# Optimization experiments

Measured on AMD Instinct MI355X. Metric: run time of the kernel, lower is better.

Reference implementation:

```python
import math
import jax, jax.numpy as jnp
import numpy as np

B, T, C = 2, 2048, 1024
N_HEAD = 16
HEAD_DIM = C // N_HEAD

def setup_inputs() -> dict:
    key = jax.random.key(0)
    kx, kq, kk, kv, kp = jax.random.split(key, 5)
    s = 1.0 / math.sqrt(C)
    return {
        "x": jax.random.normal(kx, (B, T, C), dtype=jnp.float32),
        "Wq": jax.random.normal(kq, (C, C), dtype=jnp.float32) * s,
        "Wk": jax.random.normal(kk, (C, C), dtype=jnp.float32) * s,
        "Wv": jax.random.normal(kv, (C, C), dtype=jnp.float32) * s,
        "Wproj": jax.random.normal(kp, (C, C), dtype=jnp.float32) * s,
    }

def reference(x, Wq, Wk, Wv, Wproj):
    b, t, c = x.shape
    # nn.Linear(no bias): x @ W.T ; weights stored [out, in]
    def heads(w):
        return (x @ w.T).reshape(b, t, N_HEAD, HEAD_DIM).transpose(0, 2, 1, 3)  # [B,H,T,D]
    q, k, v = heads(Wq), heads(Wk), heads(Wv)
    att = jnp.einsum('bhqd,bhkd->bhqk', q, k) / math.sqrt(HEAD_DIM)  # [B,H,T,T]
    causal = jnp.tril(jnp.ones((t, t), dtype=bool))
    att = jnp.where(causal, att, -jnp.inf)
    att = jax.nn.softmax(att, axis=-1)
    y = jnp.einsum('bhqk,bhkd->bhqd', att, v)           # [B,H,T,D]
    y = y.transpose(0, 2, 1, 3).reshape(b, t, c)        # [B,T,C]
    return y @ Wproj.T
```

## Files before the change

kernel.cpp:

```cpp
#include <hip/hip_runtime.h>
#include <stdint.h>

typedef uint16_t u16;
typedef uint32_t u32;
typedef __attribute__((ext_vector_type(8))) _Float16 f16x8;
typedef __attribute__((ext_vector_type(4))) float f32x4;

#define NB 2
#define NT 2048
#define NC 1024
#define NH 16
#define ND 64
#define NM (NB*NT)
#define LOG2E 1.44269504088896340736f

__device__ __forceinline__ u16 f2h(float f) {
  _Float16 h = (_Float16)f;
  return __builtin_bit_cast(u16, h);
}

__global__ __launch_bounds__(256) void cvt_kernel(const float* __restrict__ src,
                                                  u16* __restrict__ dst, int n4) {
  int i = blockIdx.x * 256 + threadIdx.x;
  if (i >= n4) return;
  float4 v = ((const float4*)src)[i];
  ushort4 o;
  o.x = f2h(v.x); o.y = f2h(v.y); o.z = f2h(v.z); o.w = f2h(v.w);
  ((ushort4*)dst)[i] = o;
}

__global__ __launch_bounds__(256) void cvtw_kernel(const float* __restrict__ w0,
                                                   const float* __restrict__ w1,
                                                   const float* __restrict__ w2,
                                                   const float* __restrict__ w3,
                                                   u16* __restrict__ dst) {
  int i = blockIdx.x * 256 + threadIdx.x;
  int which = i >> 18;
  const float* src = (which == 0) ? w0 : (which == 1) ? w1 : (which == 2) ? w2 : w3;
  int j = i & 262143;
  float4 v = ((const float4*)src)[j];
  ushort4 o;
  o.x = f2h(v.x); o.y = f2h(v.y); o.z = f2h(v.z); o.w = f2h(v.w);
  ((ushort4*)dst)[i] = o;
}

__device__ __forceinline__ void gload16(const void* g, void* l) {
  __builtin_amdgcn_global_load_lds(
      (const __attribute__((address_space(1))) void*)g,
      (__attribute__((address_space(3))) void*)l, 16, 0, 0);
}

template<int EPI>
__global__ __launch_bounds__(256) void gemm_bt(const u16* __restrict__ A,
                                               const u16* __restrict__ Bw,
                                               int K, int N,
                                               u16* __restrict__ oq, u16* __restrict__ okk,
                                               u16* __restrict__ ovt,
                                               float* __restrict__ of) {
  __shared__ __align__(16) u16 SH[2*128*64];
  u16* Al = SH;
  u16* Bl = SH + 128*64;
  const int tid = threadIdx.x, lane = tid & 63, wid = tid >> 6;
  const int g = lane >> 4, qq = lane & 15;
  const int wm = wid >> 1, wn = wid & 1;
  const int m0 = blockIdx.y * 128, n0 = blockIdx.x * 128;
  const int srow = lane >> 3;
  const int scol = (lane & 7) * 8;

  f32x4 acc[4][4] = {};

  for (int kt = 0; kt < K; kt += 64) {
    #pragma unroll
    for (int pp = 0; pp < 4; ++pp) {
      int r = wid*32 + pp*8;
      gload16(A  + (size_t)(m0 + r + srow)*K + kt + scol, &Al[r*64]);
      gload16(Bw + (size_t)(n0 + r + srow)*K + kt + scol, &Bl[r*64]);
    }
    __syncthreads();
    #pragma unroll
    for (int kk = 0; kk < 2; ++kk) {
      f16x8 af[4], bfr[4];
      #pragma unroll
      for (int mt = 0; mt < 4; ++mt)
        af[mt] = *(const f16x8*)&Al[(wm*64 + mt*16 + qq)*64 + kk*32 + 8*g];
      #pragma unroll
      for (int nt = 0; nt < 4; ++nt)
        bfr[nt] = *(const f16x8*)&Bl[(wn*64 + nt*16 + qq)*64 + kk*32 + 8*g];
      #pragma unroll
      for (int mt = 0; mt < 4; ++mt)
        #pragma unroll
        for (int nt = 0; nt < 4; ++nt)
          acc[mt][nt] = __builtin_amdgcn_mfma_f32_16x16x32_f16(af[mt], bfr[nt], acc[mt][nt], 0, 0, 0);
    }
    __syncthreads();
  }

  if (EPI == 0) {
    u16* reg = SH + wid*4096;
    const int sel = n0 >> 10;
    const int h = ((n0 & 1023) >> 6) + wn;
    const int bq = m0 >> 11;

    if (sel < 2) {
      const float scale = (sel == 0) ? 0.125f*LOG2E : 1.0f;
      #pragma unroll
      for (int mt = 0; mt < 4; ++mt)
        #pragma unroll
        for (int r = 0; r < 4; ++r) {
          int mloc = mt*16 + g*4 + r;
          #pragma unroll
          for (int nt = 0; nt < 4; ++nt) {
            int d = nt*16 + qq;
            reg[mloc*64 + (d ^ (g << 4))] = f2h(acc[mt][nt][r] * scale);
          }
        }
      u16* dst = (sel == 0) ? oq : okk;
      const int slot = lane & 7;
      #pragma unroll
      for (int i = 0; i < 8; ++i) {
        int row = i*8 + (lane >> 3);
        int physslot = slot ^ (((row >> 2) & 3) << 1);
        f16x8 vvv = *(const f16x8*)&reg[row*64 + physslot*8];
        int m = m0 + wm*64 + row;
        int t = m & (NT-1);
        *(f16x8*)(dst + (((size_t)(bq*NH + h)*NT + t)*ND) + slot*8) = vvv;
      }
    } else {
      #pragma unroll
      for (int nt = 0; nt < 4; ++nt) {
        int d = nt*16 + qq;
        int f = (d & 7) << 3;
        #pragma unroll
        for (int mt = 0; mt < 4; ++mt)
          #pragma unroll
          for (int rp = 0; rp < 2; ++rp) {
            int r = rp*2;
            int mloc = mt*16 + g*4 + r;
            u32 pk = (u32)f2h(acc[mt][nt][r]) | ((u32)f2h(acc[mt][nt][r+1]) << 16);
            *(u32*)&reg[d*64 + (mloc ^ f)] = pk;
          }
      }
      const int slot = lane & 7;
      const int t0 = m0 + wm*64;
      #pragma unroll
      for (int i = 0; i < 8; ++i) {
        int d = i*8 + (lane >> 3);
        int physslot = slot ^ (d & 7);
        f16x8 vvv = *(const f16x8*)&reg[d*64 + physslot*8];
        int t = (t0 & (NT-1)) + slot*8;
        *(f16x8*)(ovt + ((size_t)(bq*NH + h)*ND + d)*NT + t) = vvv;
      }
    }
  } else {
    #pragma unroll
    for (int mt = 0; mt < 4; ++mt)
      #pragma unroll
      for (int r = 0; r < 4; ++r) {
        int m = m0 + wm*64 + mt*16 + g*4 + r;
        #pragma unroll
        for (int nt = 0; nt < 4; ++nt) {
          int n = n0 + wn*64 + nt*16 + qq;
          of[(size_t)m*N + n] = acc[mt][nt][r];
        }
      }
  }
}

__global__ __launch_bounds__(256) void attn_kernel(const u16* __restrict__ q,
                                                   const u16* __restrict__ k,
                                                   const u16* __restrict__ vt,
                                                   u16* __restrict__ y) {
  __shared__ __align__(16) u16 Kl[2][64*64];
  __shared__ __align__(16) u16 Vl[2][64*64];
  __shared__ __align__(16) u16 Pl[4*16*64];
  const int tid = threadIdx.x, lane = tid & 63, wid = tid >> 6;
  const int g = lane >> 4, qq = lane & 15;
  const int bh = blockIdx.x;
  const int yy = blockIdx.y;
  const int hmap4[4] = {0, 31, 8, 23};
  const int qtile = yy ^ hmap4[yy >> 3];
  const int qs = qtile * 64;
  const u16* qp = q  + (size_t)bh*NT*ND;
  const u16* kp = k  + (size_t)bh*NT*ND;
  const u16* vp = vt + (size_t)bh*ND*NT;
  const int b = bh >> 4, h = bh & 15;
  const int srow = lane >> 3;
  const int scol8 = (lane & 7) ^ (srow & 7);
  u16* pl = &Pl[wid*1024];
  u32* plw = (u32*)pl;

  f16x8 aq[2];
  {
    int t = qs + wid*16 + qq;
    #pragma unroll
    for (int c = 0; c < 2; ++c)
      aq[c] = *(const f16x8*)(qp + (size_t)t*ND + c*32 + 8*g);
  }

  f32x4 accO[4] = {};
  float m_run = -1e30f, ssum = 0.f;

  const int ntiles = qtile + 1;

  #pragma unroll
  for (int pp = 0; pp < 2; ++pp) {
    int issue = wid*2 + pp;
    int row = issue*8 + srow;
    gload16(kp + (size_t)row*ND + scol8*8, &Kl[0][issue*512]);
    gload16(vp + (size_t)row*NT + scol8*8, &Vl[0][issue*512]);
  }

  for (int kt = 0; kt < ntiles; ++kt) {
    const int kvs = kt*64;
    const int cur = kt & 1;
    __syncthreads();

    if (kt + 1 < ntiles) {
      const int kvs2 = kvs + 64;
      #pragma unroll
      for (int pp = 0; pp < 2; ++pp) {
        int issue = wid*2 + pp;
        int row = issue*8 + srow;
        gload16(kp + (size_t)(kvs2 + row)*ND + scol8*8, &Kl[cur^1][issue*512]);
        gload16(vp + (size_t)row*NT + kvs2 + scol8*8, &Vl[cur^1][issue*512]);
      }
    }

    f32x4 sacc[4] = {};
    __builtin_amdgcn_s_setprio(1);
    #pragma unroll
    for (int c = 0; c < 2; ++c) {
      #pragma unroll
      for (int nt = 0; nt < 4; ++nt) {
        int row = nt*16 + qq;
        int col = (c*32 + 8*g) ^ ((row & 7) << 3);
        f16x8 kb = *(const f16x8*)&Kl[cur][row*64 + col];
        sacc[nt] = __builtin_amdgcn_mfma_f32_16x16x32_f16(kb, aq[c], sacc[nt], 0, 0, 0);
      }
    }
    __builtin_amdgcn_s_setprio(0);

    if (kvs + 63 > qs + wid*16) {
      int qg = qs + wid*16 + qq;
      #pragma unroll
      for (int nt = 0; nt < 4; ++nt)
        #pragma unroll
        for (int r = 0; r < 4; ++r)
          if (kvs + nt*16 + g*4 + r > qg) sacc[nt][r] = -1e30f;
    }

    float mloc = sacc[0][0];
    #pragma unroll
    for (int nt = 0; nt < 4; ++nt)
      #pragma unroll
      for (int r = 0; r < 4; ++r) mloc = fmaxf(mloc, sacc[nt][r]);
    mloc = fmaxf(mloc, __shfl_xor(mloc, 16));
    mloc = fmaxf(mloc, __shfl_xor(mloc, 32));

    const bool defer = __all(mloc <= m_run + 8.f);
    float mnew = defer ? m_run : fmaxf(m_run, mloc);

    float p[4][4];
    float ps = 0.f;
    #pragma unroll
    for (int nt = 0; nt < 4; ++nt)
      #pragma unroll
      for (int r = 0; r < 4; ++r) {
        float e = exp2f(sacc[nt][r] - mnew);
        p[nt][r] = e; ps += e;
      }
    ps += __shfl_xor(ps, 16);
    ps += __shfl_xor(ps, 32);

    if (defer) {
      ssum += ps;
    } else {
      float a = exp2f(m_run - mnew);
      ssum = ssum*a + ps;
      m_run = mnew;
      #pragma unroll
      for (int r = 0; r < 4; ++r) {
        float ar = __shfl(a, (lane & 48) + g*4 + r);
        #pragma unroll
        for (int nt = 0; nt < 4; ++nt) accO[nt][r] *= ar;
      }
    }

    #pragma unroll
    for (int nt = 0; nt < 4; ++nt)
      #pragma unroll
      for (int t2 = 0; t2 < 2; ++t2) {
        u32 pk = __builtin_bit_cast(u32,
                   __builtin_amdgcn_cvt_pkrtz(p[nt][2*t2], p[nt][2*t2+1]));
        int kv = nt*16 + g*4 + 2*t2;
        plw[(qq*64 + (kv ^ ((qq & 7) << 3))) >> 1] = pk;
      }

    __builtin_amdgcn_s_setprio(1);
    #pragma unroll
    for (int c = 0; c < 2; ++c) {
      f16x8 pa = *(const f16x8*)&pl[qq*64 + ((c*32 + 8*g) ^ ((qq & 7) << 3))];
      #pragma unroll
      for (int nt = 0; nt < 4; ++nt) {
        int vrow = nt*16 + qq;
        int vcol = (c*32 + 8*g) ^ ((vrow & 7) << 3);
        f16x8 vb = *(const f16x8*)&Vl[cur][vrow*64 + vcol];
        accO[nt] = __builtin_amdgcn_mfma_f32_16x16x32_f16(pa, vb, accO[nt], 0, 0, 0);
      }
    }
    __builtin_amdgcn_s_setprio(0);
  }

  float inv = 1.0f / ssum;
  #pragma unroll
  for (int r = 0; r < 4; ++r) {
    float invr = __shfl(inv, (lane & 48) + g*4 + r);
    int t = qs + wid*16 + g*4 + r;
    #pragma unroll
    for (int nt = 0; nt < 4; ++nt) {
      int d = nt*16 + qq;
      y[((size_t)(b*NT + t))*NC + h*ND + d] = f2h(accO[nt][r] * invr);
    }
  }
}

extern "C" void kernel_launch(void* const* d_in, const int* in_sizes, int n_in,
                              void* d_out, int out_size, void* d_ws, size_t ws_size,
                              hipStream_t stream) {
  const float* x  = (const float*)d_in[0];
  const float* Wq = (const float*)d_in[1];
  const float* Wk = (const float*)d_in[2];
  const float* Wv = (const float*)d_in[3];
  const float* Wp = (const float*)d_in[4];

  u16* xb   = (u16*)d_ws;
  u16* wqkv = xb   + (size_t)NM*NC;
  u16* wpj  = wqkv + (size_t)3*NC*NC;
  u16* qb   = wpj  + (size_t)NC*NC;
  u16* kb   = qb   + (size_t)NM*NC;
  u16* vtb  = kb   + (size_t)NM*NC;
  u16* yb   = vtb  + (size_t)NM*NC;
  size_t need = ((size_t)NM*NC*5 + (size_t)4*NC*NC) * sizeof(u16);
  if (ws_size < need) return;

  cvt_kernel<<<NM*NC/4/256, 256, 0, stream>>>(x, xb, NM*NC/4);
  cvtw_kernel<<<4*NC*NC/4/256, 256, 0, stream>>>(Wq, Wk, Wv, Wp, wqkv);

  gemm_bt<0><<<dim3(3*NC/128, NM/128), 256, 0, stream>>>(xb, wqkv, NC, 3*NC,
                                                         qb, kb, vtb, nullptr);
  attn_kernel<<<dim3(NB*NH, 32), 256, 0, stream>>>(qb, kb, vtb, yb);
  gemm_bt<1><<<dim3(NC/128, NM/128), 256, 0, stream>>>(yb, wpj, NC, NC,
                                                       nullptr, nullptr, nullptr,
                                                       (float*)d_out);
}
```

Baseline: 138.3 us.

## Compute softmax row sums via MFMA with ones and drop balanced qtile mapping

Replaces the per-tile shuffle-reduced softmax denominator with an extra MFMA that multiplies the fp16 P tile by a ones vector, accumulating row sums alongside the output. The cross-lane max reduction is moved inside the non-deferred branch, so it only runs when the running max must be rescaled. The grid is also reordered to put q-tiles on blockIdx.x, which drops the XOR-based load-balancing map, so causal work order changes. The changes cut shuffles and VALU reductions but add an MFMA per chunk and sum fp16-rounded probabilities. The deferred path now tests each lane's partial row max in __all instead of the full row max; this looks equivalent, since the wave-wide __all covers all lanes.

Measured after the change: 158.6 us. 14.7% more time.

```diff
diff --git a/kernel.cpp b/kernel.cpp
--- a/kernel.cpp
+++ b/kernel.cpp
@@ -175,10 +175,8 @@
   __shared__ __align__(16) u16 Pl[4*16*64];
   const int tid = threadIdx.x, lane = tid & 63, wid = tid >> 6;
   const int g = lane >> 4, qq = lane & 15;
-  const int bh = blockIdx.x;
-  const int yy = blockIdx.y;
-  const int hmap4[4] = {0, 31, 8, 23};
-  const int qtile = yy ^ hmap4[yy >> 3];
+  const int qtile = blockIdx.x;
+  const int bh = blockIdx.y;
   const int qs = qtile * 64;
   const u16* qp = q  + (size_t)bh*NT*ND;
   const u16* kp = k  + (size_t)bh*NT*ND;
@@ -197,8 +195,13 @@
       aq[c] = *(const f16x8*)(qp + (size_t)t*ND + c*32 + 8*g);
   }
 
+  f16x8 vones;
+  #pragma unroll
+  for (int i = 0; i < 8; ++i) vones[i] = (_Float16)1.0f;
+
   f32x4 accO[4] = {};
-  float m_run = -1e30f, ssum = 0.f;
+  f32x4 accS = {};
+  float m_run = -1e30f;
 
   const int ntiles = qtile + 1;
 
@@ -249,57 +252,49 @@
           if (kvs + nt*16 + g*4 + r > qg) sacc[nt][r] = -1e30f;
     }
 
-    float mloc = sacc[0][0];
-    #pragma unroll
-    for (int nt = 0; nt < 4; ++nt)
-      #pragma unroll
-      for (int r = 0; r < 4; ++r) mloc = fmaxf(mloc, sacc[nt][r]);
-    mloc = fmaxf(mloc, __shfl_xor(mloc, 16));
-    mloc = fmaxf(mloc, __shfl_xor(mloc, 32));
+    float m0a = fmaxf(fmaxf(sacc[0][0], sacc[0][1]), fmaxf(sacc[0][2], sacc[0][3]));
+    float m1a = fmaxf(fmaxf(sacc[1][0], sacc[1][1]), fmaxf(sacc[1][2], sacc[1][3]));
+    float m2a = fmaxf(fmaxf(sacc[2][0], sacc[2][1]), fmaxf(sacc[2][2], sacc[2][3]));
+    float m3a = fmaxf(fmaxf(sacc[3][0], sacc[3][1]), fmaxf(sacc[3][2], sacc[3][3]));
+    float mloc = fmaxf(fmaxf(m0a, m1a), fmaxf(m2a, m3a));
 
     const bool defer = __all(mloc <= m_run + 8.f);
-    float mnew = defer ? m_run : fmaxf(m_run, mloc);
-
-    float p[4][4];
-    float ps = 0.f;
-    #pragma unroll
-    for (int nt = 0; nt < 4; ++nt)
-      #pragma unroll
-      for (int r = 0; r < 4; ++r) {
-        float e = exp2f(sacc[nt][r] - mnew);
-        p[nt][r] = e; ps += e;
-      }
-    ps += __shfl_xor(ps, 16);
-    ps += __shfl_xor(ps, 32);
-
+    float mnew;
     if (defer) {
-      ssum += ps;
+      mnew = m_run;
     } else {
+      float mf = fmaxf(mloc, __shfl_xor(mloc, 16));
+      mf = fmaxf(mf, __shfl_xor(mf, 32));
+      mnew = fmaxf(m_run, mf);
       float a = exp2f(m_run - mnew);
-      ssum = ssum*a + ps;
       m_run = mnew;
       #pragma unroll
       for (int r = 0; r < 4; ++r) {
         float ar = __shfl(a, (lane & 48) + g*4 + r);
         #pragma unroll
         for (int nt = 0; nt < 4; ++nt) accO[nt][r] *= ar;
-      }
-    }
-
-    #pragma unroll
-    for (int nt = 0; nt < 4; ++nt)
-      #pragma unroll
-      for (int t2 = 0; t2 < 2; ++t2) {
-        u32 pk = __builtin_bit_cast(u32,
-                   __builtin_amdgcn_cvt_pkrtz(p[nt][2*t2], p[nt][2*t2+1]));
-        int kv = nt*16 + g*4 + 2*t2;
-        plw[(qq*64 + (kv ^ ((qq & 7) << 3))) >> 1] = pk;
-      }
+        accS[r] *= ar;
+      }
+    }
+
+    #pragma unroll
+    for (int nt = 0; nt < 4; ++nt) {
+      float p0 = exp2f(sacc[nt][0] - mnew);
+      float p1 = exp2f(sacc[nt][1] - mnew);
+      float p2 = exp2f(sacc[nt][2] - mnew);
+      float p3 = exp2f(sacc[nt][3] - mnew);
+      u32 pk0 = __builtin_bit_cast(u32, __builtin_amdgcn_cvt_pkrtz(p0, p1));
+      u32 pk1 = __builtin_bit_cast(u32, __builtin_amdgcn_cvt_pkrtz(p2, p3));
+      int kv0 = nt*16 + g*4;
+      plw[(qq*64 + (kv0 ^ ((qq & 7) << 3))) >> 1] = pk0;
+      plw[(qq*64 + ((kv0 + 2) ^ ((qq & 7) << 3))) >> 1] = pk1;
+    }
 
     __builtin_amdgcn_s_setprio(1);
     #pragma unroll
     for (int c = 0; c < 2; ++c) {
       f16x8 pa = *(const f16x8*)&pl[qq*64 + ((c*32 + 8*g) ^ ((qq & 7) << 3))];
+      accS = __builtin_amdgcn_mfma_f32_16x16x32_f16(pa, vones, accS, 0, 0, 0);
       #pragma unroll
       for (int nt = 0; nt < 4; ++nt) {
         int vrow = nt*16 + qq;
@@ -311,10 +306,9 @@
     __builtin_amdgcn_s_setprio(0);
   }
 
-  float inv = 1.0f / ssum;
   #pragma unroll
   for (int r = 0; r < 4; ++r) {
-    float invr = __shfl(inv, (lane & 48) + g*4 + r);
+    float invr = 1.0f / accS[r];
     int t = qs + wid*16 + g*4 + r;
     #pragma unroll
     for (int nt = 0; nt < 4; ++nt) {
@@ -348,7 +342,7 @@
 
   gemm_bt<0><<<dim3(3*NC/128, NM/128), 256, 0, stream>>>(xb, wqkv, NC, 3*NC,
                                                          qb, kb, vtb, nullptr);
-  attn_kernel<<<dim3(NB*NH, 32), 256, 0, stream>>>(qb, kb, vtb, yb);
+  attn_kernel<<<dim3(32, NB*NH), 256, 0, stream>>>(qb, kb, vtb, yb);
   gemm_bt<1><<<dim3(NC/128, NM/128), 256, 0, stream>>>(yb, wpj, NC, NC,
                                                        nullptr, nullptr, nullptr,
                                                        (float*)d_out);
```
